# Kernel tuning notes

Measured on AMD Instinct MI355X. Metric: run time of the kernel, lower is better.

## Reference

```python
import jax, jax.numpy as jnp
import numpy as np

NUM_GROUPS = 8
INPUT_DIM = 1024
OUTPUT_DIM = 1024
TOKENS_PER_GROUP = 8192  # rows per group after reshape


def setup_inputs() -> dict:
    key = jax.random.key(0)
    kx, kw = jax.random.split(key)
    # x: [N*G, D_in] as fed to the torch module (it reshapes internally)
    x = jax.random.normal(kx, (TOKENS_PER_GROUP * NUM_GROUPS, INPUT_DIM), dtype=jnp.float32)
    # Stacked per-group Linear weights, torch layout [D_out, D_in] per group.
    # Xavier-normal gain=1: std = sqrt(2 / (fan_in + fan_out))
    std = np.sqrt(2.0 / (INPUT_DIM + OUTPUT_DIM)).astype(np.float32)
    W = jax.random.normal(kw, (NUM_GROUPS, OUTPUT_DIM, INPUT_DIM), dtype=jnp.float32) * std
    return {"x": x, "W": W}


def reference(x, W):
    # x: [N*G, D_in] -> [N, G, D_in]
    n = x.shape[0] // NUM_GROUPS
    xg = x.reshape(n, NUM_GROUPS, INPUT_DIM)
    # per-group linear: out[n,g,k] = sum_d xg[n,g,d] * W[g,k,d]
    out = jnp.einsum("ngd,gkd->ngk", xg, W)
    return out.reshape(-1, OUTPUT_DIM)
```

## Files before the change

### kernel.cpp

```cpp
#include <hip/hip_runtime.h>
#include <hip/hip_bf16.h>


namespace {

constexpr int NG   = 8;
constexpr int DIN  = 1024;
constexpr int DOUT = 1024;
constexpr int BM   = 256;
constexpr int BN   = 256;
constexpr int BK   = 64;
constexpr int NKT  = DIN / BK;
constexpr int ROWB = BK * 2;
constexpr int TILE = BM * ROWB;
constexpr int LDS_BYTES = 4 * TILE;
constexpr int JTN  = DOUT / BN;
constexpr size_t WSB_BYTES = (size_t)NG * JTN * NKT * TILE;

typedef __attribute__((ext_vector_type(8))) short bf16x8;
typedef __attribute__((ext_vector_type(4))) float f32x4;

__device__ __forceinline__ bf16x8 pack_bf16x8v(f32x4 lo, f32x4 hi) {
  union { __hip_bfloat162 h2[4]; bf16x8 v; } p;
  p.h2[0] = __float22bfloat162_rn(make_float2(lo.x, lo.y));
  p.h2[1] = __float22bfloat162_rn(make_float2(lo.z, lo.w));
  p.h2[2] = __float22bfloat162_rn(make_float2(hi.x, hi.y));
  p.h2[3] = __float22bfloat162_rn(make_float2(hi.z, hi.w));
  return p.v;
}

__device__ __forceinline__ void glds16(const void* g, void* l) {
  __builtin_amdgcn_global_load_lds(
      (const __attribute__((address_space(1))) unsigned int*)g,
      (__attribute__((address_space(3))) unsigned int*)l, 16, 0, 0);
}

#define FENCE() asm volatile("" ::: "memory")
#define BAR()   do { FENCE(); __builtin_amdgcn_s_barrier(); FENCE(); } while (0)
#define LGKM0() asm volatile("s_waitcnt lgkmcnt(0)" ::: "memory")
#define VM0()   asm volatile("s_waitcnt vmcnt(0)" ::: "memory")
#define VMC16() asm volatile("s_waitcnt vmcnt(16)" ::: "memory")
#define MFMA_(a, b, c) __builtin_amdgcn_mfma_f32_16x16x32_bf16((a), (b), (c), 0, 0, 0)

__global__ __launch_bounds__(256)
void cvt_w_kernel(const float* __restrict__ W, char* __restrict__ wsB) {
  const int q    = (int)blockIdx.x * 256 + (int)threadIdx.x;
  const int tile = q >> 13;
  const int q13  = q & 8191;
  const int r    = q13 >> 5;
  const int cp   = q13 & 31;
  const int g    = tile >> 6;
  const int jt   = (tile >> 4) & 3;
  const int kt   = tile & 15;

  const float2 s = *(const float2*)(
      W + ((size_t)(g * DOUT + jt * BN + r)) * DIN + kt * 64 + 2 * cp);
  union { __hip_bfloat162 h; unsigned u; } pk;
  pk.h = __float22bfloat162_rn(make_float2(s.x, s.y));

  const int swzr = (r & 7) << 4;
  const int dstByte = r * ROWB + (((cp >> 2) * 16) ^ swzr) + (cp & 3) * 4;
  *(unsigned*)(wsB + (size_t)tile * TILE + dstByte) = pk.u;
}

#define ISSUE_A(TT, CUR)                                                       \
  { const float* Ai = aSrc + (size_t)(TT) * BK;                                \
    _Pragma("unroll")                                                          \
    for (int p = 0; p < 8; ++p) {                                              \
      aL[CUR][2 * p]     = *(const f32x4*)(Ai + p * ARSTR);                    \
      aL[CUR][2 * p + 1] = *(const f32x4*)(Ai + p * ARSTR + 4);                \
    } }

#define WRITE_A(CUR, DBUF)                                                     \
  { _Pragma("unroll")                                                          \
    for (int p = 0; p < 8; ++p)                                                \
      *(bf16x8*)((DBUF) + dst0 + p * 4096) =                                   \
          pack_bf16x8v(aL[CUR][2 * p], aL[CUR][2 * p + 1]); }

#define PBODY(T, CUR)                                                          \
  {                                                                            \
    char* const nA = smA + (((T) + 1) & 1) * TILE;                             \
    char* const nB = smB + (((T) + 1) & 1) * TILE;                             \
    const char* Bi = BgT + (size_t)((T) + 1) * TILE;                           \
    _Pragma("unroll")                                                          \
    for (int p = 0; p < 8; ++p)                     \
      glds16(Bi + dst0 + p * 4096, nB + dst0 + p * 4096);                      \
    FENCE();                                                                   \
    if ((T) + 2 < NKT) ISSUE_A((T) + 2, CUR);                                  \
    FENCE();                                                                   \
    WRITE_A((CUR) ^ 1, nA);                    \
    LGKM0();                                                                   \
    if ((T) + 2 < NKT) { VMC16(); } else { VM0(); }                            \
    BAR();                                                                     \
  }

template <bool WSB>
__global__ __launch_bounds__(768, 3)
void gemm_ws(const float* __restrict__ X, const float* __restrict__ W,
             const char* __restrict__ wsB, float* __restrict__ O) {
  extern __shared__ char smem[];
  char* const smA = smem;
  char* const smB = smem + 2 * TILE;

  const int bid = (int)blockIdx.x;
  const int swz = (bid & 7) * 128 + (bid >> 3);
  const int jt = swz & 3;
  const int it = (swz >> 2) & 31;
  const int g  = swz >> 7;

  const int n0 = it * BM;
  const int c0 = jt * BN;

  const int tid  = (int)threadIdx.x;
  const int lane = tid & 63;
  const int wid  = tid >> 6;

  if (wid < 8) {
    const int wr = (wid >> 2) & 1;
    const int wc = wid & 3;
    const int fr = lane & 15;
    const int fq = lane >> 4;
    const int colx0 = ((fq       ^ (fr & 7)) << 4);
    const int colx1 = (((4 + fq) ^ (fr & 7)) << 4);
    const int aRow0 = (wr * 128 + fr) * ROWB;
    const int bRow0 = (wc * 64  + fr) * ROWB;

    f32x4 acc[8][4];
#pragma unroll
    for (int m = 0; m < 8; ++m)
#pragma unroll
      for (int n = 0; n < 4; ++n) acc[m][n] = (f32x4){0.f, 0.f, 0.f, 0.f};

    BAR();

    for (int t = 0; t < NKT; ++t) {
      char* const cA = smA + (t & 1) * TILE;
      char* const cB = smB + (t & 1) * TILE;
#pragma unroll
      for (int ks = 0; ks < 2; ++ks) {
        const int cx = ks ? colx1 : colx0;
        bf16x8 bfr[4];
#pragma unroll
        for (int n = 0; n < 4; ++n)
          bfr[n] = *(const bf16x8*)(cB + bRow0 + n * 2048 + cx);
        __builtin_amdgcn_s_setprio(1);
#pragma unroll
        for (int m = 0; m < 8; ++m) {
          bf16x8 am = *(const bf16x8*)(cA + aRow0 + m * 2048 + cx);
#pragma unroll
          for (int n = 0; n < 4; ++n)
            acc[m][n] = MFMA_(am, bfr[n], acc[m][n]);
        }
        __builtin_amdgcn_s_setprio(0);
      }
      if (t + 1 < NKT) BAR();
    }

#pragma unroll
    for (int m = 0; m < 8; ++m) {
#pragma unroll
      for (int r = 0; r < 4; ++r) {
        const int row = wr * 128 + m * 16 + fq * 4 + r;
        float* orow = O + ((size_t)(n0 + row) * NG + g) * DOUT + c0 + wc * 64;
#pragma unroll
        for (int n = 0; n < 4; ++n) {
          orow[n * 16 + fr] = acc[m][n][r];
        }
      }
    }
  } else {
    const int ptid = tid - 512;
    const int r0   = ptid >> 3;
    const int sl   = ptid & 7;
    const int lg   = sl ^ (r0 & 7);
    const int dst0 = ptid * 16;

    const float* aSrc = X + ((size_t)(n0 + r0) * NG + g) * DIN + lg * 8;
    constexpr size_t ARSTR = (size_t)32 * NG * DIN;
    const char* BgT = wsB + (size_t)((g * JTN + jt) * NKT) * TILE;
    const float* bSrc = W + ((size_t)(g * DOUT + c0 + r0)) * DIN + lg * 8;
    constexpr size_t BRSTR = (size_t)32 * DIN;

    f32x4 aL[2][16];

    if (WSB) {
#pragma unroll
      for (int p = 0; p < 8; ++p)
        glds16(BgT + dst0 + p * 4096, smB + dst0 + p * 4096);
      FENCE();
      ISSUE_A(0, 0);
      ISSUE_A(1, 1);
      FENCE();
      WRITE_A(0, smA);
      LGKM0();
      BAR();

      for (int tt = 0; tt + 1 < NKT; tt += 2) {
        PBODY(tt, 0);
        if (tt + 2 < NKT) PBODY(tt + 1, 1);
      }
    } else {
      f32x4 bL[16];
#pragma unroll
      for (int p = 0; p < 8; ++p) {
        aL[0][2 * p]     = *(const f32x4*)(aSrc + p * ARSTR);
        aL[0][2 * p + 1] = *(const f32x4*)(aSrc + p * ARSTR + 4);
        bL[2 * p]        = *(const f32x4*)(bSrc + p * BRSTR);
        bL[2 * p + 1]    = *(const f32x4*)(bSrc + p * BRSTR + 4);
      }
      WRITE_A(0, smA);
#pragma unroll
      for (int p = 0; p < 8; ++p)
        *(bf16x8*)(smB + dst0 + p * 4096) =
            pack_bf16x8v(bL[2 * p], bL[2 * p + 1]);
      LGKM0();
      BAR();
      for (int t = 0; t + 1 < NKT; ++t) {
        char* const nA = smA + ((t + 1) & 1) * TILE;
        char* const nB = smB + ((t + 1) & 1) * TILE;
        const float* Ai = aSrc + (size_t)(t + 1) * BK;
        const float* Bi = bSrc + (size_t)(t + 1) * BK;
#pragma unroll
        for (int p = 0; p < 8; ++p) {
          aL[0][2 * p]     = *(const f32x4*)(Ai + p * ARSTR);
          aL[0][2 * p + 1] = *(const f32x4*)(Ai + p * ARSTR + 4);
          bL[2 * p]        = *(const f32x4*)(Bi + p * BRSTR);
          bL[2 * p + 1]    = *(const f32x4*)(Bi + p * BRSTR + 4);
        }
        WRITE_A(0, nA);
#pragma unroll
        for (int p = 0; p < 8; ++p)
          *(bf16x8*)(nB + dst0 + p * 4096) =
              pack_bf16x8v(bL[2 * p], bL[2 * p + 1]);
        LGKM0();
        BAR();
      }
    }
  }
}

}

extern "C" void kernel_launch(void* const* d_in, const int* in_sizes, int n_in,
                              void* d_out, int out_size, void* d_ws, size_t ws_size,
                              hipStream_t stream) {
  (void)n_in; (void)out_size;
  const float* X = (const float*)d_in[0];
  const float* W = (const float*)d_in[1];
  float* O = (float*)d_out;

  const int tokens_total = in_sizes[0] / DIN;
  const int ntok_per_g   = tokens_total / NG;
  const int grid = NG * (ntok_per_g / BM) * (DOUT / BN);

  if (ws_size >= WSB_BYTES) {
    const int cvt_grid = (int)(WSB_BYTES / 4 / 256);
    cvt_w_kernel<<<dim3(cvt_grid), dim3(256), 0, stream>>>(W, (char*)d_ws);
    (void)hipFuncSetAttribute((const void*)gemm_ws<true>,
                              hipFuncAttributeMaxDynamicSharedMemorySize,
                              LDS_BYTES);
    gemm_ws<true><<<dim3(grid), dim3(768), LDS_BYTES, stream>>>(
        X, W, (const char*)d_ws, O);
  } else {
    (void)hipFuncSetAttribute((const void*)gemm_ws<false>,
                              hipFuncAttributeMaxDynamicSharedMemorySize,
                              LDS_BYTES);
    gemm_ws<false><<<dim3(grid), dim3(768), LDS_BYTES, stream>>>(
        X, W, nullptr, O);
  }
}
```

Baseline: 213.2 us.

## Pre-pack weights in MFMA fragment order and load B directly into registers

The weight conversion kernel now writes bf16 weights in per-lane MFMA fragment order, so the compute waves can load their B fragments straight from global memory into registers. This removes the B tile from LDS, the global-to-LDS copies and the LDS reads of B, and halves the shared memory per block. Each compute wave prefetches the next k-tile's B fragments after the current MFMAs. The risk is global-load latency landing on the MFMA critical path, and duplicated B reads across waves that share a column tile (the two row halves).

```diff
diff --git a/kernel.cpp b/kernel.cpp
--- a/kernel.cpp
+++ b/kernel.cpp
@@ -13,9 +13,9 @@
 constexpr int NKT  = DIN / BK;
 constexpr int ROWB = BK * 2;
 constexpr int TILE = BM * ROWB;
-constexpr int LDS_BYTES = 4 * TILE;
 constexpr int JTN  = DOUT / BN;
-constexpr size_t WSB_BYTES = (size_t)NG * JTN * NKT * TILE;
+constexpr int FRAGT = 32 * 1024;
+constexpr size_t WSB_BYTES = (size_t)NG * JTN * NKT * FRAGT;
 
 typedef __attribute__((ext_vector_type(8))) short bf16x8;
 typedef __attribute__((ext_vector_type(4))) float f32x4;
@@ -29,38 +29,30 @@
   return p.v;
 }
 
-__device__ __forceinline__ void glds16(const void* g, void* l) {
-  __builtin_amdgcn_global_load_lds(
-      (const __attribute__((address_space(1))) unsigned int*)g,
-      (__attribute__((address_space(3))) unsigned int*)l, 16, 0, 0);
-}
-
 #define FENCE() asm volatile("" ::: "memory")
 #define BAR()   do { FENCE(); __builtin_amdgcn_s_barrier(); FENCE(); } while (0)
 #define LGKM0() asm volatile("s_waitcnt lgkmcnt(0)" ::: "memory")
-#define VM0()   asm volatile("s_waitcnt vmcnt(0)" ::: "memory")
-#define VMC16() asm volatile("s_waitcnt vmcnt(16)" ::: "memory")
 #define MFMA_(a, b, c) __builtin_amdgcn_mfma_f32_16x16x32_bf16((a), (b), (c), 0, 0, 0)
 
 __global__ __launch_bounds__(256)
 void cvt_w_kernel(const float* __restrict__ W, char* __restrict__ wsB) {
   const int q    = (int)blockIdx.x * 256 + (int)threadIdx.x;
-  const int tile = q >> 13;
-  const int q13  = q & 8191;
-  const int r    = q13 >> 5;
-  const int cp   = q13 & 31;
+  const int tile = q >> 11;
+  const int f2   = (q >> 6) & 31;
+  const int l    = q & 63;
   const int g    = tile >> 6;
   const int jt   = (tile >> 4) & 3;
   const int kt   = tile & 15;
-
-  const float2 s = *(const float2*)(
-      W + ((size_t)(g * DOUT + jt * BN + r)) * DIN + kt * 64 + 2 * cp);
-  union { __hip_bfloat162 h; unsigned u; } pk;
-  pk.h = __float22bfloat162_rn(make_float2(s.x, s.y));
-
-  const int swzr = (r & 7) << 4;
-  const int dstByte = r * ROWB + (((cp >> 2) * 16) ^ swzr) + (cp & 3) * 4;
-  *(unsigned*)(wsB + (size_t)tile * TILE + dstByte) = pk.u;
+  const int wc   = f2 >> 3;
+  const int n    = (f2 >> 1) & 3;
+  const int ks   = f2 & 1;
+
+  const int row = jt * BN + wc * 64 + n * 16 + (l & 15);
+  const int col = kt * BK + ks * 32 + (l >> 4) * 8;
+  const float* src = W + (size_t)(g * DOUT + row) * DIN + col;
+  f32x4 lo = *(const f32x4*)(src);
+  f32x4 hi = *(const f32x4*)(src + 4);
+  *(bf16x8*)(wsB + (size_t)q * 16) = pack_bf16x8v(lo, hi);
 }
 
 #define ISSUE_A(TT, CUR)                                                       \
@@ -76,23 +68,6 @@
     for (int p = 0; p < 8; ++p)                                                \
       *(bf16x8*)((DBUF) + dst0 + p * 4096) =                                   \
           pack_bf16x8v(aL[CUR][2 * p], aL[CUR][2 * p + 1]); }
-
-#define PBODY(T, CUR)                                                          \
-  {                                                                            \
-    char* const nA = smA + (((T) + 1) & 1) * TILE;                             \
-    char* const nB = smB + (((T) + 1) & 1) * TILE;                             \
-    const char* Bi = BgT + (size_t)((T) + 1) * TILE;                           \
-    _Pragma("unroll")                                                          \
-    for (int p = 0; p < 8; ++p)                     \
-      glds16(Bi + dst0 + p * 4096, nB + dst0 + p * 4096);                      \
-    FENCE();                                                                   \
-    if ((T) + 2 < NKT) ISSUE_A((T) + 2, CUR);                                  \
-    FENCE();                                                                   \
-    WRITE_A((CUR) ^ 1, nA);                    \
-    LGKM0();                                                                   \
-    if ((T) + 2 < NKT) { VMC16(); } else { VM0(); }                            \
-    BAR();                                                                     \
-  }
 
 template <bool WSB>
 __global__ __launch_bounds__(768, 3)
@@ -125,11 +100,23 @@
     const int aRow0 = (wr * 128 + fr) * ROWB;
     const int bRow0 = (wc * 64  + fr) * ROWB;
 
+    const char* BgF = wsB + (size_t)((g * JTN + jt) * NKT) * FRAGT
+                          + (size_t)wc * 8 * 1024 + lane * 16;
+
     f32x4 acc[8][4];
 #pragma unroll
     for (int m = 0; m < 8; ++m)
 #pragma unroll
       for (int n = 0; n < 4; ++n) acc[m][n] = (f32x4){0.f, 0.f, 0.f, 0.f};
+
+    bf16x8 bfr[4][2];
+    if (WSB) {
+#pragma unroll
+      for (int n = 0; n < 4; ++n)
+#pragma unroll
+        for (int ks = 0; ks < 2; ++ks)
+          bfr[n][ks] = *(const bf16x8*)(BgF + (n * 2 + ks) * 1024);
+    }
 
     BAR();
 
@@ -139,19 +126,28 @@
 #pragma unroll
       for (int ks = 0; ks < 2; ++ks) {
         const int cx = ks ? colx1 : colx0;
-        bf16x8 bfr[4];
-#pragma unroll
-        for (int n = 0; n < 4; ++n)
-          bfr[n] = *(const bf16x8*)(cB + bRow0 + n * 2048 + cx);
+        if (!WSB) {
+#pragma unroll
+          for (int n = 0; n < 4; ++n)
+            bfr[n][ks] = *(const bf16x8*)(cB + bRow0 + n * 2048 + cx);
+        }
         __builtin_amdgcn_s_setprio(1);
 #pragma unroll
         for (int m = 0; m < 8; ++m) {
           bf16x8 am = *(const bf16x8*)(cA + aRow0 + m * 2048 + cx);
 #pragma unroll
           for (int n = 0; n < 4; ++n)
-            acc[m][n] = MFMA_(am, bfr[n], acc[m][n]);
+            acc[m][n] = MFMA_(am, bfr[n][ks], acc[m][n]);
         }
         __builtin_amdgcn_s_setprio(0);
+      }
+      if (WSB && t + 1 < NKT) {
+        const char* Bn = BgF + (size_t)(t + 1) * FRAGT;
+#pragma unroll
+        for (int n = 0; n < 4; ++n)
+#pragma unroll
+          for (int ks = 0; ks < 2; ++ks)
+            bfr[n][ks] = *(const bf16x8*)(Bn + (n * 2 + ks) * 1024);
       }
       if (t + 1 < NKT) BAR();
     }
@@ -177,17 +173,12 @@
 
     const float* aSrc = X + ((size_t)(n0 + r0) * NG + g) * DIN + lg * 8;
     constexpr size_t ARSTR = (size_t)32 * NG * DIN;
-    const char* BgT = wsB + (size_t)((g * JTN + jt) * NKT) * TILE;
     const float* bSrc = W + ((size_t)(g * DOUT + c0 + r0)) * DIN + lg * 8;
     constexpr size_t BRSTR = (size_t)32 * DIN;
 
     f32x4 aL[2][16];
 
     if (WSB) {
-#pragma unroll
-      for (int p = 0; p < 8; ++p)
-        glds16(BgT + dst0 + p * 4096, smB + dst0 + p * 4096);
-      FENCE();
       ISSUE_A(0, 0);
       ISSUE_A(1, 1);
       FENCE();
@@ -195,9 +186,14 @@
       LGKM0();
       BAR();
 
-      for (int tt = 0; tt + 1 < NKT; tt += 2) {
-        PBODY(tt, 0);
-        if (tt + 2 < NKT) PBODY(tt + 1, 1);
+      for (int t = 0; t + 1 < NKT; ++t) {
+        char* const nA = smA + ((t + 1) & 1) * TILE;
+        const int cur = t & 1;
+        if (t + 2 < NKT) ISSUE_A(t + 2, cur);
+        FENCE();
+        WRITE_A(cur ^ 1, nA);
+        LGKM0();
+        BAR();
       }
     } else {
       f32x4 bL[16];
@@ -254,18 +250,18 @@
   const int grid = NG * (ntok_per_g / BM) * (DOUT / BN);
 
   if (ws_size >= WSB_BYTES) {
-    const int cvt_grid = (int)(WSB_BYTES / 4 / 256);
+    const int cvt_grid = (int)(WSB_BYTES / 16 / 256);
     cvt_w_kernel<<<dim3(cvt_grid), dim3(256), 0, stream>>>(W, (char*)d_ws);
+    const int lds = 2 * TILE;
     (void)hipFuncSetAttribute((const void*)gemm_ws<true>,
-                              hipFuncAttributeMaxDynamicSharedMemorySize,
-                              LDS_BYTES);
-    gemm_ws<true><<<dim3(grid), dim3(768), LDS_BYTES, stream>>>(
+                              hipFuncAttributeMaxDynamicSharedMemorySize, lds);
+    gemm_ws<true><<<dim3(grid), dim3(768), lds, stream>>>(
         X, W, (const char*)d_ws, O);
   } else {
+    const int lds = 4 * TILE;
     (void)hipFuncSetAttribute((const void*)gemm_ws<false>,
-                              hipFuncAttributeMaxDynamicSharedMemorySize,
-                              LDS_BYTES);
-    gemm_ws<false><<<dim3(grid), dim3(768), LDS_BYTES, stream>>>(
+                              hipFuncAttributeMaxDynamicSharedMemorySize, lds);
+    gemm_ws<false><<<dim3(grid), dim3(768), lds, stream>>>(
         X, W, nullptr, O);
   }
 }
```

New measurement: 588.4 us. +176.0%, slower.
